# Kernel tuning notes

Measured on AMD Instinct MI355X. Metric: run time of the kernel, lower is better.

The kernel has to match this reference:

```python
import jax, jax.numpy as jnp
import numpy as np

B, SQ, SK, DK, DV = 16, 2048, 2048, 64, 64


def setup_inputs() -> dict:
    key = jax.random.key(0)
    kq, kk, kv, km = jax.random.split(key, 4)
    Q = jax.random.normal(kq, (B, SQ, DK), dtype=jnp.float32)
    K = jax.random.normal(kk, (B, SK, DK), dtype=jnp.float32)
    V = jax.random.normal(kv, (B, SK, DV), dtype=jnp.float32)
    mask = jax.random.randint(km, (B, 1, SK), 0, 2, dtype=jnp.int32)
    return {"Q": Q, "K": K, "V": V, "mask": mask}


def reference(Q, K, V, mask):
    d = K.shape[-1]
    # scores: (B, SQ, SK) -- full attention matrix, as in the torch module
    attn = jnp.einsum("bqd,bkd->bqk", Q, K) / (d ** 0.5)
    masked = mask == 0  # (B, 1, SK), broadcasts over query dim
    attn = jnp.where(masked, jnp.float32(-1e9), attn)
    attn = jax.nn.softmax(attn, axis=-1)
    attn = jnp.where(masked, jnp.float32(0.0), attn)
    output = jnp.einsum("bqk,bkv->bqv", attn, V)
    return (output, attn)
```

## Files before the change

### kernel.cpp

```cpp
#include <hip/hip_runtime.h>

#define NB   16
#define SQL  2048
#define SKL  2048
#define DKL  64
#define DVL  64
#define NE   (NB * SQL * DKL)

typedef __attribute__((ext_vector_type(8))) short short8;
typedef __attribute__((ext_vector_type(4))) short s16x4;
typedef __attribute__((ext_vector_type(4))) float f32x4;

#define PST 56

#define SCALE_LOG2E 0.1803368801111204f
#define EXP2F(x) __builtin_amdgcn_exp2f(x)

__device__ __forceinline__ short f2bf(float x) {
    unsigned u = __builtin_bit_cast(unsigned, x);
    u = (u + 0x7fffu + ((u >> 16) & 1u)) >> 16;
    return (short)u;
}
__device__ __forceinline__ float bf2f(short s) {
    return __builtin_bit_cast(float, ((unsigned)(unsigned short)s) << 16);
}

__global__ __launch_bounds__(256)
void prep(const float* __restrict__ Q, const float* __restrict__ K,
          short* __restrict__ ws)
{
    short* qhi = ws;
    short* qlo = ws + (size_t)NE;
    short* khi = ws + (size_t)2 * NE;
    short* klo = ws + (size_t)3 * NE;

    size_t i4 = ((size_t)blockIdx.x * 256 + threadIdx.x) * 4;
    if (i4 >= NE) return;

    f32x4 q = *(const f32x4*)(Q + i4);
    f32x4 k = *(const f32x4*)(K + i4);
    s16x4 qh, ql, kh, kl;
    #pragma unroll
    for (int j = 0; j < 4; j++) {
        qh[j] = f2bf(q[j]);  ql[j] = f2bf(q[j] - bf2f(qh[j]));
        kh[j] = f2bf(k[j]);  kl[j] = f2bf(k[j] - bf2f(kh[j]));
    }
    *(s16x4*)(qhi + i4) = qh;
    *(s16x4*)(qlo + i4) = ql;
    *(s16x4*)(khi + i4) = kh;
    *(s16x4*)(klo + i4) = kl;
}

__global__ __launch_bounds__(256)
void vtrans(const float* __restrict__ V, short* __restrict__ vt)
{
    __shared__ short st[64][72];
    const int b  = blockIdx.x >> 5;
    const int kt = blockIdx.x & 31;
    const int t  = threadIdx.x;

    const int kr = t >> 2;
    const int c0 = (t & 3) * 16;
    const float* vsrc = V + ((size_t)(b * SKL) + kt * 64 + kr) * DVL + c0;
    #pragma unroll
    for (int j = 0; j < 4; j++) {
        f32x4 x = *(const f32x4*)(vsrc + j * 4);
        #pragma unroll
        for (int i = 0; i < 4; i++) st[kr][c0 + j * 4 + i] = f2bf(x[i]);
    }
    __syncthreads();

    const int vr = t >> 2;
    const int k0 = (t & 3) * 16;
    short* dst = vt + (size_t)b * DVL * SKL + (size_t)vr * SKL + kt * 64 + k0;
    #pragma unroll
    for (int j = 0; j < 4; j++) {
        s16x4 o;
        #pragma unroll
        for (int m = 0; m < 4; m++) o[m] = st[k0 + j * 4 + m][vr];
        *(s16x4*)(dst + j * 4) = o;
    }
}

__device__ __forceinline__ void qk_tiles(const short* __restrict__ khi,
                                         const short* __restrict__ klo, int kb,
                                         int l15, int quad,
                                         short8 qa0h, short8 qa1h,
                                         short8 qa0l, short8 qa1l,
                                         f32x4& s0, f32x4& s1) {
    size_t o0 = (size_t)(kb + l15) * DKL + quad * 8;
    size_t o1 = (size_t)(kb + 16 + l15) * DKL + quad * 8;
    short8 h0l = *(const short8*)(khi + o0);
    short8 h0h = *(const short8*)(khi + o0 + 32);
    short8 h1l = *(const short8*)(khi + o1);
    short8 h1h = *(const short8*)(khi + o1 + 32);
    short8 l0l = *(const short8*)(klo + o0);
    short8 l0h = *(const short8*)(klo + o0 + 32);
    short8 l1l = *(const short8*)(klo + o1);
    short8 l1h = *(const short8*)(klo + o1 + 32);
    f32x4 z = {0.f, 0.f, 0.f, 0.f};
    s0 = __builtin_amdgcn_mfma_f32_16x16x32_bf16(qa0h, h0l, z, 0, 0, 0);
    s0 = __builtin_amdgcn_mfma_f32_16x16x32_bf16(qa1h, h0h, s0, 0, 0, 0);
    s0 = __builtin_amdgcn_mfma_f32_16x16x32_bf16(qa0h, l0l, s0, 0, 0, 0);
    s0 = __builtin_amdgcn_mfma_f32_16x16x32_bf16(qa1h, l0h, s0, 0, 0, 0);
    s0 = __builtin_amdgcn_mfma_f32_16x16x32_bf16(qa0l, h0l, s0, 0, 0, 0);
    s0 = __builtin_amdgcn_mfma_f32_16x16x32_bf16(qa1l, h0h, s0, 0, 0, 0);
    s1 = __builtin_amdgcn_mfma_f32_16x16x32_bf16(qa0h, h1l, z, 0, 0, 0);
    s1 = __builtin_amdgcn_mfma_f32_16x16x32_bf16(qa1h, h1h, s1, 0, 0, 0);
    s1 = __builtin_amdgcn_mfma_f32_16x16x32_bf16(qa0h, l1l, s1, 0, 0, 0);
    s1 = __builtin_amdgcn_mfma_f32_16x16x32_bf16(qa1h, l1h, s1, 0, 0, 0);
    s1 = __builtin_amdgcn_mfma_f32_16x16x32_bf16(qa0l, h1l, s1, 0, 0, 0);
    s1 = __builtin_amdgcn_mfma_f32_16x16x32_bf16(qa1l, h1h, s1, 0, 0, 0);
}

__global__ __launch_bounds__(256, 4)
void attn_fwd(const short* __restrict__ ws, const int* __restrict__ mask,
              float* __restrict__ out, float* __restrict__ attn)
{
    __shared__ __align__(16) char smem[16384 + 256];
    short* s_p   = (short*)smem;
    f32x4* s_acc = (f32x4*)smem;
    float* s_red = (float*)(smem + 16384);

    const int tid  = threadIdx.x;
    const int w    = tid >> 6;
    const int lane = tid & 63;
    const int l15  = tid & 15;
    const int quad = (tid & 63) >> 4;

    const int bid = blockIdx.x;
    const int swz = (bid & 7) * ((NB * SQL / 16) >> 3) + (bid >> 3);
    const int b     = swz >> 7;
    const int qbase = (swz & 127) * 16;

    const int k0 = w * (SKL / 4);
    const int k1 = k0 + SKL / 4;

    const short* qhi = ws + (size_t)(b * SQL + qbase) * DKL;
    const short* qlo = qhi + (size_t)NE;
    const short* khi = ws + (size_t)2 * NE + (size_t)b * SKL * DKL;
    const short* klo = khi + (size_t)NE;
    const short* vtg = ws + (size_t)4 * NE + (size_t)b * DVL * SKL;
    const int*   mk  = mask + b * SKL;

    short8 qa0h = *(const short8*)(qhi + (size_t)l15 * DKL + quad * 8);
    short8 qa1h = *(const short8*)(qhi + (size_t)l15 * DKL + 32 + quad * 8);
    short8 qa0l = *(const short8*)(qlo + (size_t)l15 * DKL + quad * 8);
    short8 qa1l = *(const short8*)(qlo + (size_t)l15 * DKL + 32 + quad * 8);

    float lsum[4] = {0.f, 0.f, 0.f, 0.f};
    for (int kb = k0; kb < k1; kb += 32) {
        f32x4 s0, s1;
        qk_tiles(khi, klo, kb, l15, quad, qa0h, qa1h, qa0l, qa1l, s0, s1);
        float bias0 = mk[kb + l15]      ? 0.0f : -1e9f;
        float bias1 = mk[kb + 16 + l15] ? 0.0f : -1e9f;
        #pragma unroll
        for (int r = 0; r < 4; r++) {
            lsum[r] += EXP2F(fmaf(s0[r], SCALE_LOG2E, bias0));
            lsum[r] += EXP2F(fmaf(s1[r], SCALE_LOG2E, bias1));
        }
    }
    #pragma unroll
    for (int off = 1; off <= 8; off <<= 1) {
        #pragma unroll
        for (int r = 0; r < 4; r++)
            lsum[r] += __shfl_xor(lsum[r], off, 64);
    }
    if (l15 == 0) {
        #pragma unroll
        for (int r = 0; r < 4; r++) s_red[w * 16 + quad * 4 + r] = lsum[r];
    }
    __syncthreads();
    float inv_l[4];
    #pragma unroll
    for (int r = 0; r < 4; r++) {
        float t_ = s_red[quad * 4 + r] + s_red[16 + quad * 4 + r]
                 + s_red[32 + quad * 4 + r] + s_red[48 + quad * 4 + r];
        inv_l[r] = 1.0f / t_;
    }

    f32x4 acc[4];
    #pragma unroll
    for (int vt = 0; vt < 4; vt++) { f32x4 z = {0.f,0.f,0.f,0.f}; acc[vt] = z; }

    short* pw = s_p + w * 16 * PST;

    for (int kb = k0; kb < k1; kb += 32) {
        const short* vrow = vtg + kb + quad * 8;
        short8 bv0 = *(const short8*)(vrow + (size_t)(0 * 16 + l15) * SKL);
        short8 bv1 = *(const short8*)(vrow + (size_t)(1 * 16 + l15) * SKL);
        short8 bv2 = *(const short8*)(vrow + (size_t)(2 * 16 + l15) * SKL);
        short8 bv3 = *(const short8*)(vrow + (size_t)(3 * 16 + l15) * SKL);
        float bias0 = mk[kb + l15]      ? 0.0f : -1e9f;
        float bias1 = mk[kb + 16 + l15] ? 0.0f : -1e9f;

        f32x4 s0, s1;
        qk_tiles(khi, klo, kb, l15, quad, qa0h, qa1h, qa0l, qa1l, s0, s1);

        const size_t arow = (size_t)(b * SQL + qbase + quad * 4) * SKL + kb;
        #pragma unroll
        for (int r = 0; r < 4; r++) {
            float p0 = EXP2F(fmaf(s0[r], SCALE_LOG2E, bias0)) * inv_l[r];
            float p1 = EXP2F(fmaf(s1[r], SCALE_LOG2E, bias1)) * inv_l[r];
            __builtin_nontemporal_store(p0, &attn[arow + (size_t)r * SKL + l15]);
            __builtin_nontemporal_store(p1, &attn[arow + (size_t)r * SKL + 16 + l15]);
            pw[(quad * 4 + r) * PST + l15]      = f2bf(p0);
            pw[(quad * 4 + r) * PST + 16 + l15] = f2bf(p1);
        }

        short8 pa = *(const short8*)(pw + l15 * PST + quad * 8);
        acc[0] = __builtin_amdgcn_mfma_f32_16x16x32_bf16(pa, bv0, acc[0], 0, 0, 0);
        acc[1] = __builtin_amdgcn_mfma_f32_16x16x32_bf16(pa, bv1, acc[1], 0, 0, 0);
        acc[2] = __builtin_amdgcn_mfma_f32_16x16x32_bf16(pa, bv2, acc[2], 0, 0, 0);
        acc[3] = __builtin_amdgcn_mfma_f32_16x16x32_bf16(pa, bv3, acc[3], 0, 0, 0);
    }

    __syncthreads();
    #pragma unroll
    for (int vt = 0; vt < 4; vt++) s_acc[(w * 64 + lane) * 4 + vt] = acc[vt];
    __syncthreads();

    f32x4 t_ = s_acc[(0 * 64 + lane) * 4 + w];
    #pragma unroll
    for (int wp = 1; wp < 4; wp++) {
        f32x4 u = s_acc[(wp * 64 + lane) * 4 + w];
        #pragma unroll
        for (int r = 0; r < 4; r++) t_[r] += u[r];
    }
    #pragma unroll
    for (int r = 0; r < 4; r++)
        out[(size_t)(b * SQL + qbase + quad * 4 + r) * DVL + w * 16 + l15] = t_[r];
}

extern "C" void kernel_launch(void* const* d_in, const int* in_sizes, int n_in,
                              void* d_out, int out_size, void* d_ws, size_t ws_size,
                              hipStream_t stream) {
    const float* Q    = (const float*)d_in[0];
    const float* K    = (const float*)d_in[1];
    const float* V    = (const float*)d_in[2];
    const int*   mask = (const int*)d_in[3];
    float* out  = (float*)d_out;
    float* attn = out + (size_t)NB * SQL * DVL;
    short* ws   = (short*)d_ws;

    prep<<<dim3(NE / (256 * 4)), dim3(256), 0, stream>>>(Q, K, ws);
    vtrans<<<dim3(NB * (SKL / 64)), dim3(256), 0, stream>>>(V, ws + (size_t)4 * NE);
    attn_fwd<<<dim3(NB * (SQL / 16)), dim3(256), 0, stream>>>(ws, mask, out, attn);
}
```

Before: 550.8 us.

## Transpose score MFMA so P stays in registers, feeding PV without LDS

Swaps the A/B operands of the QK^T MFMAs so each lane holds four consecutive key columns of one query row. The P fragment can then be packed directly into a bf16 MFMA operand with v_cvt_pk_bf16_f32, and V^T is pre-permuted in the prep kernel to match. This removes the LDS round-trip for P and allows 16-byte vectorized nontemporal attn stores and vectorized mask loads. It also folds 1/l into the exponent as a log2 bias, and splits the score MFMA chain into two independent accumulators for more ILP. In exchange it adds extra VALU adds and depends on the bf16 rounding of the packed conversion.

Result: no change. 558.7 us (+1.4%).

```diff
diff --git a/kernel.cpp b/kernel.cpp
--- a/kernel.cpp
+++ b/kernel.cpp
@@ -10,11 +10,12 @@
 typedef __attribute__((ext_vector_type(8))) short short8;
 typedef __attribute__((ext_vector_type(4))) short s16x4;
 typedef __attribute__((ext_vector_type(4))) float f32x4;
-
-#define PST 56
+typedef __attribute__((ext_vector_type(4))) int   i32x4;
+typedef __attribute__((ext_vector_type(4))) unsigned u32x4;
 
 #define SCALE_LOG2E 0.1803368801111204f
 #define EXP2F(x) __builtin_amdgcn_exp2f(x)
+#define MFMA32(a,b,c) __builtin_amdgcn_mfma_f32_16x16x32_bf16((a),(b),(c),0,0,0)
 
 __device__ __forceinline__ short f2bf(float x) {
     unsigned u = __builtin_bit_cast(unsigned, x);
@@ -23,6 +24,16 @@
 }
 __device__ __forceinline__ float bf2f(short s) {
     return __builtin_bit_cast(float, ((unsigned)(unsigned short)s) << 16);
+}
+
+__device__ __forceinline__ short8 pk8(f32x4 a, f32x4 b) {
+    unsigned w0, w1, w2, w3;
+    asm("v_cvt_pk_bf16_f32 %0, %1, %2" : "=v"(w0) : "v"(a[0]), "v"(a[1]));
+    asm("v_cvt_pk_bf16_f32 %0, %1, %2" : "=v"(w1) : "v"(a[2]), "v"(a[3]));
+    asm("v_cvt_pk_bf16_f32 %0, %1, %2" : "=v"(w2) : "v"(b[0]), "v"(b[1]));
+    asm("v_cvt_pk_bf16_f32 %0, %1, %2" : "=v"(w3) : "v"(b[2]), "v"(b[3]));
+    u32x4 t = {w0, w1, w2, w3};
+    return __builtin_bit_cast(short8, t);
 }
 
 __global__ __launch_bounds__(256)
@@ -71,46 +82,21 @@
     __syncthreads();
 
     const int vr = t >> 2;
-    const int k0 = (t & 3) * 16;
-    short* dst = vt + (size_t)b * DVL * SKL + (size_t)vr * SKL + kt * 64 + k0;
-    #pragma unroll
-    for (int j = 0; j < 4; j++) {
-        s16x4 o;
-        #pragma unroll
-        for (int m = 0; m < 4; m++) o[m] = st[k0 + j * 4 + m][vr];
-        *(s16x4*)(dst + j * 4) = o;
-    }
-}
-
-__device__ __forceinline__ void qk_tiles(const short* __restrict__ khi,
-                                         const short* __restrict__ klo, int kb,
-                                         int l15, int quad,
-                                         short8 qa0h, short8 qa1h,
-                                         short8 qa0l, short8 qa1l,
-                                         f32x4& s0, f32x4& s1) {
-    size_t o0 = (size_t)(kb + l15) * DKL + quad * 8;
-    size_t o1 = (size_t)(kb + 16 + l15) * DKL + quad * 8;
-    short8 h0l = *(const short8*)(khi + o0);
-    short8 h0h = *(const short8*)(khi + o0 + 32);
-    short8 h1l = *(const short8*)(khi + o1);
-    short8 h1h = *(const short8*)(khi + o1 + 32);
-    short8 l0l = *(const short8*)(klo + o0);
-    short8 l0h = *(const short8*)(klo + o0 + 32);
-    short8 l1l = *(const short8*)(klo + o1);
-    short8 l1h = *(const short8*)(klo + o1 + 32);
-    f32x4 z = {0.f, 0.f, 0.f, 0.f};
-    s0 = __builtin_amdgcn_mfma_f32_16x16x32_bf16(qa0h, h0l, z, 0, 0, 0);
-    s0 = __builtin_amdgcn_mfma_f32_16x16x32_bf16(qa1h, h0h, s0, 0, 0, 0);
-    s0 = __builtin_amdgcn_mfma_f32_16x16x32_bf16(qa0h, l0l, s0, 0, 0, 0);
-    s0 = __builtin_amdgcn_mfma_f32_16x16x32_bf16(qa1h, l0h, s0, 0, 0, 0);
-    s0 = __builtin_amdgcn_mfma_f32_16x16x32_bf16(qa0l, h0l, s0, 0, 0, 0);
-    s0 = __builtin_amdgcn_mfma_f32_16x16x32_bf16(qa1l, h0h, s0, 0, 0, 0);
-    s1 = __builtin_amdgcn_mfma_f32_16x16x32_bf16(qa0h, h1l, z, 0, 0, 0);
-    s1 = __builtin_amdgcn_mfma_f32_16x16x32_bf16(qa1h, h1h, s1, 0, 0, 0);
-    s1 = __builtin_amdgcn_mfma_f32_16x16x32_bf16(qa0h, l1l, s1, 0, 0, 0);
-    s1 = __builtin_amdgcn_mfma_f32_16x16x32_bf16(qa1h, l1h, s1, 0, 0, 0);
-    s1 = __builtin_amdgcn_mfma_f32_16x16x32_bf16(qa0l, h1l, s1, 0, 0, 0);
-    s1 = __builtin_amdgcn_mfma_f32_16x16x32_bf16(qa1l, h1h, s1, 0, 0, 0);
+    const int cc = (t & 3) * 16;
+    short* dst = vt + (size_t)b * DVL * SKL + (size_t)vr * SKL + kt * 64 + cc;
+    short o[16];
+    #pragma unroll
+    for (int m = 0; m < 16; m++) {
+        int kk = cc + m;
+        int tb = kk >> 5;
+        int w5 = kk & 31;
+        int qd = w5 >> 3;
+        int jj = w5 & 7;
+        int kl = tb * 32 + qd * 4 + (jj & 3) + ((jj >> 2) << 4);
+        o[m] = st[kl][vr];
+    }
+    *(short8*)(dst)     = *(short8*)(o);
+    *(short8*)(dst + 8) = *(short8*)(o + 8);
 }
 
 __global__ __launch_bounds__(256, 4)
@@ -118,7 +104,6 @@
               float* __restrict__ out, float* __restrict__ attn)
 {
     __shared__ __align__(16) char smem[16384 + 256];
-    short* s_p   = (short*)smem;
     f32x4* s_acc = (f32x4*)smem;
     float* s_red = (float*)(smem + 16384);
 
@@ -148,74 +133,104 @@
     short8 qa0l = *(const short8*)(qlo + (size_t)l15 * DKL + quad * 8);
     short8 qa1l = *(const short8*)(qlo + (size_t)l15 * DKL + 32 + quad * 8);
 
-    float lsum[4] = {0.f, 0.f, 0.f, 0.f};
+    float lsum = 0.f;
     for (int kb = k0; kb < k1; kb += 32) {
-        f32x4 s0, s1;
-        qk_tiles(khi, klo, kb, l15, quad, qa0h, qa1h, qa0l, qa1l, s0, s1);
-        float bias0 = mk[kb + l15]      ? 0.0f : -1e9f;
-        float bias1 = mk[kb + 16 + l15] ? 0.0f : -1e9f;
+        size_t o0 = (size_t)(kb + l15) * DKL + quad * 8;
+        size_t o1 = o0 + (size_t)16 * DKL;
+        short8 h0l = *(const short8*)(khi + o0);
+        short8 h0h = *(const short8*)(khi + o0 + 32);
+        short8 h1l = *(const short8*)(khi + o1);
+        short8 h1h = *(const short8*)(khi + o1 + 32);
+        short8 l0l = *(const short8*)(klo + o0);
+        short8 l0h = *(const short8*)(klo + o0 + 32);
+        short8 l1l = *(const short8*)(klo + o1);
+        short8 l1h = *(const short8*)(klo + o1 + 32);
+        i32x4 m0 = *(const i32x4*)(mk + kb + quad * 4);
+        i32x4 m1 = *(const i32x4*)(mk + kb + 16 + quad * 4);
+
+        f32x4 z = {0.f, 0.f, 0.f, 0.f};
+        f32x4 sA0 = MFMA32(h0l, qa0h, z);
+        sA0 = MFMA32(l0l, qa0h, sA0);
+        sA0 = MFMA32(h0l, qa0l, sA0);
+        f32x4 sB0 = MFMA32(h0h, qa1h, z);
+        sB0 = MFMA32(l0h, qa1h, sB0);
+        sB0 = MFMA32(h0h, qa1l, sB0);
+        f32x4 sA1 = MFMA32(h1l, qa0h, z);
+        sA1 = MFMA32(l1l, qa0h, sA1);
+        sA1 = MFMA32(h1l, qa0l, sA1);
+        f32x4 sB1 = MFMA32(h1h, qa1h, z);
+        sB1 = MFMA32(l1h, qa1h, sB1);
+        sB1 = MFMA32(h1h, qa1l, sB1);
+
         #pragma unroll
         for (int r = 0; r < 4; r++) {
-            lsum[r] += EXP2F(fmaf(s0[r], SCALE_LOG2E, bias0));
-            lsum[r] += EXP2F(fmaf(s1[r], SCALE_LOG2E, bias1));
+            lsum += EXP2F(fmaf(sA0[r] + sB0[r], SCALE_LOG2E, m0[r] ? 0.f : -1e9f));
+            lsum += EXP2F(fmaf(sA1[r] + sB1[r], SCALE_LOG2E, m1[r] ? 0.f : -1e9f));
         }
     }
-    #pragma unroll
-    for (int off = 1; off <= 8; off <<= 1) {
-        #pragma unroll
-        for (int r = 0; r < 4; r++)
-            lsum[r] += __shfl_xor(lsum[r], off, 64);
-    }
-    if (l15 == 0) {
-        #pragma unroll
-        for (int r = 0; r < 4; r++) s_red[w * 16 + quad * 4 + r] = lsum[r];
-    }
+    lsum += __shfl_xor(lsum, 16, 64);
+    lsum += __shfl_xor(lsum, 32, 64);
+    if (lane < 16) s_red[w * 16 + l15] = lsum;
     __syncthreads();
-    float inv_l[4];
-    #pragma unroll
-    for (int r = 0; r < 4; r++) {
-        float t_ = s_red[quad * 4 + r] + s_red[16 + quad * 4 + r]
-                 + s_red[32 + quad * 4 + r] + s_red[48 + quad * 4 + r];
-        inv_l[r] = 1.0f / t_;
-    }
+    const float tot  = s_red[l15] + s_red[16 + l15] + s_red[32 + l15] + s_red[48 + l15];
+    const float lg2i = -__log2f(tot);
 
     f32x4 acc[4];
     #pragma unroll
     for (int vt = 0; vt < 4; vt++) { f32x4 z = {0.f,0.f,0.f,0.f}; acc[vt] = z; }
-
-    short* pw = s_p + w * 16 * PST;
 
     for (int kb = k0; kb < k1; kb += 32) {
         const short* vrow = vtg + kb + quad * 8;
-        short8 bv0 = *(const short8*)(vrow + (size_t)(0 * 16 + l15) * SKL);
-        short8 bv1 = *(const short8*)(vrow + (size_t)(1 * 16 + l15) * SKL);
-        short8 bv2 = *(const short8*)(vrow + (size_t)(2 * 16 + l15) * SKL);
-        short8 bv3 = *(const short8*)(vrow + (size_t)(3 * 16 + l15) * SKL);
-        float bias0 = mk[kb + l15]      ? 0.0f : -1e9f;
-        float bias1 = mk[kb + 16 + l15] ? 0.0f : -1e9f;
-
-        f32x4 s0, s1;
-        qk_tiles(khi, klo, kb, l15, quad, qa0h, qa1h, qa0l, qa1l, s0, s1);
-
-        const size_t arow = (size_t)(b * SQL + qbase + quad * 4) * SKL + kb;
+        short8 vv0 = *(const short8*)(vrow + (size_t)(0 * 16 + l15) * SKL);
+        short8 vv1 = *(const short8*)(vrow + (size_t)(1 * 16 + l15) * SKL);
+        short8 vv2 = *(const short8*)(vrow + (size_t)(2 * 16 + l15) * SKL);
+        short8 vv3 = *(const short8*)(vrow + (size_t)(3 * 16 + l15) * SKL);
+        i32x4 m0 = *(const i32x4*)(mk + kb + quad * 4);
+        i32x4 m1 = *(const i32x4*)(mk + kb + 16 + quad * 4);
+
+        size_t o0 = (size_t)(kb + l15) * DKL + quad * 8;
+        size_t o1 = o0 + (size_t)16 * DKL;
+        short8 h0l = *(const short8*)(khi + o0);
+        short8 h0h = *(const short8*)(khi + o0 + 32);
+        short8 h1l = *(const short8*)(khi + o1);
+        short8 h1h = *(const short8*)(khi + o1 + 32);
+        short8 l0l = *(const short8*)(klo + o0);
+        short8 l0h = *(const short8*)(klo + o0 + 32);
+        short8 l1l = *(const short8*)(klo + o1);
+        short8 l1h = *(const short8*)(klo + o1 + 32);
+
+        f32x4 z = {0.f, 0.f, 0.f, 0.f};
+        f32x4 sA0 = MFMA32(h0l, qa0h, z);
+        sA0 = MFMA32(l0l, qa0h, sA0);
+        sA0 = MFMA32(h0l, qa0l, sA0);
+        f32x4 sB0 = MFMA32(h0h, qa1h, z);
+        sB0 = MFMA32(l0h, qa1h, sB0);
+        sB0 = MFMA32(h0h, qa1l, sB0);
+        f32x4 sA1 = MFMA32(h1l, qa0h, z);
+        sA1 = MFMA32(l1l, qa0h, sA1);
+        sA1 = MFMA32(h1l, qa0l, sA1);
+        f32x4 sB1 = MFMA32(h1h, qa1h, z);
+        sB1 = MFMA32(l1h, qa1h, sB1);
+        sB1 = MFMA32(h1h, qa1l, sB1);
+
+        f32x4 p0, p1;
         #pragma unroll
         for (int r = 0; r < 4; r++) {
-            float p0 = EXP2F(fmaf(s0[r], SCALE_LOG2E, bias0)) * inv_l[r];
-            float p1 = EXP2F(fmaf(s1[r], SCALE_LOG2E, bias1)) * inv_l[r];
-            __builtin_nontemporal_store(p0, &attn[arow + (size_t)r * SKL + l15]);
-            __builtin_nontemporal_store(p1, &attn[arow + (size_t)r * SKL + 16 + l15]);
-            pw[(quad * 4 + r) * PST + l15]      = f2bf(p0);
-            pw[(quad * 4 + r) * PST + 16 + l15] = f2bf(p1);
+            p0[r] = EXP2F(fmaf(sA0[r] + sB0[r], SCALE_LOG2E, m0[r] ? lg2i : -1e9f));
+            p1[r] = EXP2F(fmaf(sA1[r] + sB1[r], SCALE_LOG2E, m1[r] ? lg2i : -1e9f));
         }
 
-        short8 pa = *(const short8*)(pw + l15 * PST + quad * 8);
-        acc[0] = __builtin_amdgcn_mfma_f32_16x16x32_bf16(pa, bv0, acc[0], 0, 0, 0);
-        acc[1] = __builtin_amdgcn_mfma_f32_16x16x32_bf16(pa, bv1, acc[1], 0, 0, 0);
-        acc[2] = __builtin_amdgcn_mfma_f32_16x16x32_bf16(pa, bv2, acc[2], 0, 0, 0);
-        acc[3] = __builtin_amdgcn_mfma_f32_16x16x32_bf16(pa, bv3, acc[3], 0, 0, 0);
-    }
-
-    __syncthreads();
+        float* arow = attn + (size_t)(b * SQL + qbase + l15) * SKL + kb + quad * 4;
+        __builtin_nontemporal_store(p0, (f32x4*)arow);
+        __builtin_nontemporal_store(p1, (f32x4*)(arow + 16));
+
+        short8 pa = pk8(p0, p1);
+        acc[0] = MFMA32(pa, vv0, acc[0]);
+        acc[1] = MFMA32(pa, vv1, acc[1]);
+        acc[2] = MFMA32(pa, vv2, acc[2]);
+        acc[3] = MFMA32(pa, vv3, acc[3]);
+    }
+
     #pragma unroll
     for (int vt = 0; vt < 4; vt++) s_acc[(w * 64 + lane) * 4 + vt] = acc[vt];
     __syncthreads();
```
